# Kernel tuning notes

Measured on AMD Instinct MI355X. Metric: run time of the kernel, lower is better.

Reference implementation:

```python
import jax, jax.numpy as jnp
import numpy as np

B, T, C, HID, K, H = 8, 1024, 512, 2048, 31, 4  # batch, time, in_chans, hidden_chans, kernel, wshare


def setup_inputs() -> dict:
    key = jax.random.key(0)
    ks = jax.random.split(key, 8)
    n = lambda k_, sh, sc: jax.random.normal(k_, sh, dtype=jnp.float32) * sc
    return {
        "x": n(ks[0], (B, T, C), 1.0),
        "Wl": n(ks[1], (H * K, C), 0.05),      # linear_weight.weight
        "bl": n(ks[2], (H * K,), 0.01),          # linear_weight.bias
        "bias": n(ks[3], (C,), 0.02),            # self.bias
        "Wc": n(ks[4], (HID, C, K), 0.01),       # pointwise_conv1.weight (O,I,K)
        "bc": n(ks[5], (HID,), 0.01),            # pointwise_conv1.bias
        "W2": n(ks[6], (C, HID), 0.01),          # w_2.weight
        "b2": n(ks[7], (C,), 0.01),              # w_2.bias
    }


def reference(x, Wl, bl, bias, Wc, bc, W2, b2):
    Bq, Tq, Cq = x.shape
    d = Cq // H  # channels per weight-share head
    # dynamic conv logits: (B,T,H,K)
    logits = (x @ Wl.T + bl).reshape(Bq, Tq, H, K)
    # banded positions: output t attends to t + j - (K-1)//2
    offs = jnp.arange(K) - (K - 1) // 2
    pos = jnp.arange(Tq)[:, None] + offs[None, :]          # (T,K)
    valid = (pos >= 0) & (pos < Tq)
    logits = jnp.where(valid[None, :, None, :], logits, -jnp.inf)
    w = jax.nn.softmax(logits, axis=-1)                     # softmax over window (matches banded softmax over T)
    # gather windowed inputs: (B,T,K,H,d)
    xg = x.reshape(Bq, Tq, H, d)[:, jnp.clip(pos, 0, Tq - 1)]
    y = jnp.einsum('bthk,btkhd->bthd', w, xg).reshape(Bq, Tq, Cq)
    # (B,C,T) + bias
    y = y.transpose(0, 2, 1) + bias[None, :, None]
    # pointwise_conv1: Conv1d(C->HID, kernel K, padding 0) -> T' = T-K+1
    z = jax.lax.conv_general_dilated(y, Wc, (1,), 'VALID',
                                     dimension_numbers=('NCH', 'OIH', 'NCH'))
    z = z + bc[None, :, None]
    z = jax.nn.selu(z.transpose(0, 2, 1))                   # (B,T',HID)
    return z @ W2.T + b2                                    # (B,T',C)
```

## Files before the change

### kernel.cpp

```cpp
#include <hip/hip_runtime.h>
#include <hip/hip_bf16.h>

typedef __attribute__((ext_vector_type(8))) short short8;
typedef __attribute__((ext_vector_type(4))) float f32x4;

#define NB 8
#define NT 1024
#define NC 512
#define NHID 2048
#define NK 31
#define NH 4
#define NTP 994
#define MROWS (NB * NTP)
#define TG 4

__device__ __forceinline__ void gload_lds16(const void* g, void* l) {
  __builtin_amdgcn_global_load_lds(
      (const __attribute__((address_space(1))) void*)g,
      (__attribute__((address_space(3))) void*)l, 16, 0, 0);
}

__global__ __launch_bounds__(256) void prep_wc(const float* __restrict__ Wc,
                                               __hip_bfloat16* __restrict__ Wt) {
  const int blk = blockIdx.x;
  const int cb = blk & 7;
  const int o0 = (blk >> 3) << 3;
  const int c0 = cb << 6;
  const int obig = o0 >> 8;
  const int orb = o0 & 255;
  __shared__ float lds[8 * 64 * NK];
  for (int ol = 0; ol < 8; ++ol) {
    const float* src = Wc + ((size_t)(o0 + ol) * NC + c0) * NK;
    for (int i = threadIdx.x; i < 64 * NK; i += 256) lds[ol * (64 * NK) + i] = src[i];
  }
  __syncthreads();
  for (int i = threadIdx.x; i < NK * 8 * 64; i += 256) {
    const int k = i >> 9;
    const int rem = i & 511;
    const int ol = rem >> 6;
    const int ci = rem & 63;
    Wt[((size_t)((obig * 8 + cb) * NK + k) << 14) + ((orb + ol) << 6) + (ci ^ (ol << 3))] =
        __float2bfloat16(lds[ol * (64 * NK) + ci * NK + k]);
  }
}

__global__ __launch_bounds__(256) void prep_w2(const float* __restrict__ W2,
                                               __hip_bfloat16* __restrict__ W2t) {
  const int i = blockIdx.x * 256 + threadIdx.x;
  if (i < 32 * 512 * 64) {
    const int oi = i & 63;
    const int c = (i >> 6) & 511;
    const int kb = i >> 15;
    const size_t dst = ((size_t)(((c >> 7) * 32 + kb) * 128 + (c & 127)) << 6) +
                       (oi ^ ((c & 7) << 3));
    W2t[dst] = __float2bfloat16(W2[(size_t)c * NHID + (kb << 6) + oi]);
  }
}

__global__ __launch_bounds__(256) void dynconv(const float* __restrict__ x,
                                               const float* __restrict__ Wl,
                                               const float* __restrict__ bl,
                                               const float* __restrict__ bias,
                                               __hip_bfloat16* __restrict__ Y) {
  const int t0 = blockIdx.x * TG;
  const int b = blockIdx.y;
  const int tid = threadIdx.x, lane = tid & 63, w = tid >> 6;
  __shared__ float xt[TG][NC];
  __shared__ float lg[TG][NH * NK];
  __shared__ float wsm[TG][NH][NK];

  for (int i = tid; i < TG * NC; i += 256) {
    const int tg = i >> 9, c = i & 511;
    xt[tg][c] = x[((size_t)b * NT + t0 + tg) * NC + c];
  }
  __syncthreads();

  for (int i = 0; i < 31; ++i) {
    const int id = (i << 2) | w;
    const float* wrow = Wl + (size_t)id * NC + (lane << 3);
    float wv[8];
#pragma unroll
    for (int u = 0; u < 8; ++u) wv[u] = wrow[u];
    const float blv = bl[id];
#pragma unroll
    for (int tg = 0; tg < TG; ++tg) {
      float s = 0.f;
#pragma unroll
      for (int u = 0; u < 8; ++u) s += xt[tg][(lane << 3) + u] * wv[u];
#pragma unroll
      for (int off = 32; off; off >>= 1) s += __shfl_xor(s, off);
      if (lane == 0) lg[tg][id] = s + blv;
    }
  }
  __syncthreads();

  if (tid < TG * NH) {
    const int tg = tid >> 2, h = tid & 3;
    const int t = t0 + tg;
    int jlo = 15 - t; if (jlo < 0) jlo = 0;
    int jhi = 1038 - t; if (jhi > 30) jhi = 30;
    float mx = -1e30f;
    for (int j = jlo; j <= jhi; ++j) mx = fmaxf(mx, lg[tg][h * NK + j]);
    float ssum = 0.f;
    for (int j = 0; j < NK; ++j) {
      const float e = (j >= jlo && j <= jhi) ? __expf(lg[tg][h * NK + j] - mx) : 0.f;
      wsm[tg][h][j] = e;
      ssum += e;
    }
    const float inv = 1.f / ssum;
    for (int j = 0; j < NK; ++j) wsm[tg][h][j] *= inv;
  }
  __syncthreads();

  const int c = tid << 1;
  const int h = c >> 7;
  const float2* x2 = (const float2*)x;
  const float bias0 = bias[c], bias1 = bias[c + 1];
#pragma unroll
  for (int tg = 0; tg < TG; ++tg) {
    const int t = t0 + tg;
    float a0 = 0.f, a1 = 0.f;
#pragma unroll
    for (int j = 0; j < NK; ++j) {
      int pos = t + j - 15;
      pos = pos < 0 ? 0 : (pos > NT - 1 ? NT - 1 : pos);
      const float wgt = wsm[tg][h][j];
      const float2 v = x2[(((size_t)b * NT + pos) << 8) + tid];
      a0 += wgt * v.x;
      a1 += wgt * v.y;
    }
    const int cs = (c & ~63) | ((c & 63) ^ ((t & 7) << 3));
    __hip_bfloat162 hv;
    hv.x = __float2bfloat16(a0 + bias0);
    hv.y = __float2bfloat16(a1 + bias1);
    *(__hip_bfloat162*)(Y + ((size_t)b * NT + t) * NC + cs) = hv;
  }
}

__global__ __launch_bounds__(512, 2) void conv_gemm(const __hip_bfloat16* __restrict__ Y,
                                                    const __hip_bfloat16* __restrict__ Wt,
                                                    const float* __restrict__ bc,
                                                    __hip_bfloat16* __restrict__ Z) {
  const int o0 = blockIdx.x << 8;
  const int t0 = blockIdx.y << 8;
  const int b = blockIdx.z;
  __shared__ __align__(16) __hip_bfloat16 Ys[288 * 64];
  __shared__ __align__(16) __hip_bfloat16 Bs[2][256 * 64];
  const int tid = threadIdx.x;
  const int lane = tid & 63, wid = tid >> 6;
  const int wr = wid >> 2, wcid = wid & 3;
  const int obig = o0 >> 8;

  f32x4 acc[8][4] = {};

  auto stageY = [&](int cb_) {
    const int c0 = cb_ << 6;
#pragma unroll
    for (int p = 0; p < 5; ++p) {
      const int i = (p << 9) + tid;
      if (i < 2304) {
        int grow = t0 + (i >> 3);
        if (grow > NT - 1) grow = NT - 1;
        gload_lds16(Y + (((size_t)b * NT + grow) << 9) + c0 + ((i & 7) << 3),
                    &Ys[i << 3]);
      }
    }
  };
  auto stageB = [&](int bufi, int s_) {
    const __hip_bfloat16* wb = Wt + (((size_t)(obig * 248 + s_)) << 14);
#pragma unroll
    for (int p = 0; p < 4; ++p) {
      const int i = (p << 9) + tid;
      gload_lds16(wb + (i << 3), &Bs[bufi][i << 3]);
    }
  };

  stageY(0);
  stageB(0, 0);

  int buf = 0;
  for (int cb = 0; cb < 8; ++cb) {
    for (int k = 0; k < NK; ++k) {
      const int s = cb * 31 + k;
      if (s < 247) {
        stageB(buf ^ 1, s + 1);
        asm volatile("s_waitcnt vmcnt(4)" ::: "memory");
      } else {
        asm volatile("s_waitcnt vmcnt(0)" ::: "memory");
      }
      __builtin_amdgcn_sched_barrier(0);
      __builtin_amdgcn_s_barrier();
      __builtin_amdgcn_sched_barrier(0);

      __builtin_amdgcn_s_setprio(1);
#pragma unroll
      for (int kk = 0; kk < 2; ++kk) {
        const int ko = (kk << 5) + ((lane >> 4) << 3);
        short8 av[8], bv[4];
#pragma unroll
        for (int m = 0; m < 8; ++m) {
          const int r2 = (wr << 7) + (m << 4) + (lane & 15) + k;
          av[m] = *(const short8*)&Ys[(r2 << 6) + (ko ^ ((r2 & 7) << 3))];
        }
#pragma unroll
        for (int n = 0; n < 4; ++n) {
          const int br = (wcid << 6) + (n << 4) + (lane & 15);
          bv[n] = *(const short8*)&Bs[buf][(br << 6) + (ko ^ ((br & 7) << 3))];
        }
#pragma unroll
        for (int m = 0; m < 8; ++m)
#pragma unroll
          for (int n = 0; n < 4; ++n)
            acc[m][n] = __builtin_amdgcn_mfma_f32_16x16x32_bf16(av[m], bv[n], acc[m][n], 0, 0, 0);
      }
      __builtin_amdgcn_s_setprio(0);

      __builtin_amdgcn_sched_barrier(0);
      __builtin_amdgcn_s_barrier();
      __builtin_amdgcn_sched_barrier(0);
      buf ^= 1;
    }
    if (cb < 7) stageY(cb + 1);
  }

  const float kS = 1.0507009873554805f;
  const float kAS = 1.7580993408473766f;
#pragma unroll
  for (int n = 0; n < 4; ++n) {
    const int col = o0 + (wcid << 6) + (n << 4) + (lane & 15);
    const float bcv = bc[col];
#pragma unroll
    for (int m = 0; m < 8; ++m) {
      const int rbase = (wr << 7) + (m << 4) + ((lane >> 4) << 2);
#pragma unroll
      for (int r = 0; r < 4; ++r) {
        const int tp = t0 + rbase + r;
        if (tp < NTP) {
          const float v = acc[m][n][r] + bcv;
          const float s = v > 0.f ? kS * v : kAS * (__expf(v) - 1.f);
          const size_t grow = (size_t)b * NTP + tp;
          const int cs = (col & ~63) | ((col & 63) ^ (((int)(grow & 7)) << 3));
          Z[grow * NHID + cs] = __float2bfloat16(s);
        }
      }
    }
  }
}

__global__ __launch_bounds__(256) void out_gemm(const __hip_bfloat16* __restrict__ Zm,
                                                const __hip_bfloat16* __restrict__ W2t,
                                                const float* __restrict__ b2,
                                                float* __restrict__ Out) {
  const int n0 = blockIdx.x << 7;
  const int m0 = blockIdx.y << 7;
  __shared__ __align__(16) __hip_bfloat16 As[128 * 64];
  __shared__ __align__(16) __hip_bfloat16 Bs[128 * 64];
  const int tid = threadIdx.x;
  const int lane = tid & 63, wid = tid >> 6;
  const int wr = wid >> 1, wc = wid & 1;

  f32x4 acc[4][4] = {};

  for (int kb = 0; kb < 32; ++kb) {
#pragma unroll
    for (int p = 0; p < 4; ++p) {
      const int i = (p << 8) + tid;
      int row = m0 + (i >> 3);
      if (row > MROWS - 1) row = MROWS - 1;
      gload_lds16(Zm + ((size_t)row << 11) + (kb << 6) + ((i & 7) << 3), &As[i << 3]);
    }
    const __hip_bfloat16* wb = W2t + ((size_t)((n0 >> 7) * 32 + kb) << 13);
#pragma unroll
    for (int p = 0; p < 4; ++p) {
      const int i = (p << 8) + tid;
      gload_lds16(wb + (i << 3), &Bs[i << 3]);
    }
    __syncthreads();
#pragma unroll
    for (int kk = 0; kk < 2; ++kk) {
      const int ko = (kk << 5) + ((lane >> 4) << 3);
      short8 av[4], bv[4];
#pragma unroll
      for (int m = 0; m < 4; ++m) {
        const int r = (wr << 6) + (m << 4) + (lane & 15);
        av[m] = *(const short8*)&As[(r << 6) + (ko ^ ((r & 7) << 3))];
      }
#pragma unroll
      for (int n = 0; n < 4; ++n) {
        const int br = (wc << 6) + (n << 4) + (lane & 15);
        bv[n] = *(const short8*)&Bs[(br << 6) + (ko ^ ((br & 7) << 3))];
      }
#pragma unroll
      for (int m = 0; m < 4; ++m)
#pragma unroll
        for (int n = 0; n < 4; ++n)
          acc[m][n] = __builtin_amdgcn_mfma_f32_16x16x32_bf16(av[m], bv[n], acc[m][n], 0, 0, 0);
    }
    __syncthreads();
  }

#pragma unroll
  for (int n = 0; n < 4; ++n) {
    const int col = n0 + (wc << 6) + (n << 4) + (lane & 15);
    const float b2v = b2[col];
#pragma unroll
    for (int m = 0; m < 4; ++m) {
      const int rbase = m0 + (wr << 6) + (m << 4) + ((lane >> 4) << 2);
#pragma unroll
      for (int r = 0; r < 4; ++r) {
        const int row = rbase + r;
        if (row < MROWS) Out[(size_t)row * NC + col] = acc[m][n][r] + b2v;
      }
    }
  }
}

extern "C" void kernel_launch(void* const* d_in, const int* in_sizes, int n_in,
                              void* d_out, int out_size, void* d_ws, size_t ws_size,
                              hipStream_t stream) {
  const float* x = (const float*)d_in[0];
  const float* Wl = (const float*)d_in[1];
  const float* bl = (const float*)d_in[2];
  const float* bias = (const float*)d_in[3];
  const float* Wc = (const float*)d_in[4];
  const float* bc = (const float*)d_in[5];
  const float* W2 = (const float*)d_in[6];
  const float* b2 = (const float*)d_in[7];
  float* out = (float*)d_out;

  char* ws = (char*)d_ws;
  __hip_bfloat16* Wt = (__hip_bfloat16*)(ws);
  __hip_bfloat16* Y = (__hip_bfloat16*)(ws + 65011712);
  __hip_bfloat16* W2t = (__hip_bfloat16*)(ws + 73400320);
  __hip_bfloat16* Z = (__hip_bfloat16*)(ws + 75497472);

  hipLaunchKernelGGL(prep_wc, dim3(2048), dim3(256), 0, stream, Wc, Wt);
  hipLaunchKernelGGL(prep_w2, dim3(4096), dim3(256), 0, stream, W2, W2t);
  hipLaunchKernelGGL(dynconv, dim3(NT / TG, NB), dim3(256), 0, stream, x, Wl, bl, bias, Y);
  hipLaunchKernelGGL(conv_gemm, dim3(NHID / 256, 4, NB), dim3(512), 0, stream, Y, Wt, bc, Z);
  hipLaunchKernelGGL(out_gemm, dim3(NC / 128, (MROWS + 127) / 128), dim3(256), 0, stream,
                     Z, W2t, b2, out);
}
```

Baseline: 707.5 us.

## Triple-buffer weight tiles and split MFMA loop into four interleaved quadrant phases

The conv GEMM moves from double to triple buffering of the weight tile, prefetching two steps ahead. Each k-step is split into four quadrant phases, each with its own LDS fragment loads, MFMA batch and barrier, and the four global-to-LDS copies of the next tile are spread across those phases. The aim is to hide global-load latency and overlap LDS reads with MFMA work while using fewer live fragment registers. In exchange it adds many more barriers per step and an extra 32KB of LDS, which may limit occupancy at two blocks per CU.

```diff
diff --git a/kernel.cpp b/kernel.cpp
--- a/kernel.cpp
+++ b/kernel.cpp
@@ -19,6 +19,18 @@
       (const __attribute__((address_space(1))) void*)g,
       (__attribute__((address_space(3))) void*)l, 16, 0, 0);
 }
+
+#define BARX()                                  \
+  do {                                          \
+    __builtin_amdgcn_sched_barrier(0);          \
+    __builtin_amdgcn_s_barrier();               \
+    __builtin_amdgcn_sched_barrier(0);          \
+  } while (0)
+#define LGKM0()                                          \
+  do {                                                   \
+    asm volatile("s_waitcnt lgkmcnt(0)" ::: "memory");   \
+    __builtin_amdgcn_sched_barrier(0);                   \
+  } while (0)
 
 __global__ __launch_bounds__(256) void prep_wc(const float* __restrict__ Wc,
                                                __hip_bfloat16* __restrict__ Wt) {
@@ -145,7 +157,7 @@
   const int t0 = blockIdx.y << 8;
   const int b = blockIdx.z;
   __shared__ __align__(16) __hip_bfloat16 Ys[288 * 64];
-  __shared__ __align__(16) __hip_bfloat16 Bs[2][256 * 64];
+  __shared__ __align__(16) __hip_bfloat16 Bsm[3][256 * 64];
   const int tid = threadIdx.x;
   const int lane = tid & 63, wid = tid >> 6;
   const int wr = wid >> 2, wcid = wid & 3;
@@ -166,59 +178,130 @@
       }
     }
   };
-  auto stageB = [&](int bufi, int s_) {
+  auto stageBc = [&](__hip_bfloat16* dst, int s_, int p) {
     const __hip_bfloat16* wb = Wt + (((size_t)(obig * 248 + s_)) << 14);
-#pragma unroll
-    for (int p = 0; p < 4; ++p) {
-      const int i = (p << 9) + tid;
-      gload_lds16(wb + (i << 3), &Bs[bufi][i << 3]);
-    }
+    const int i = (p << 9) + tid;
+    gload_lds16(wb + (i << 3), dst + (i << 3));
   };
 
+  __hip_bfloat16* b0 = Bsm[0];
+  __hip_bfloat16* b1 = Bsm[1];
+  __hip_bfloat16* b2 = Bsm[2];
+
   stageY(0);
-  stageB(0, 0);
-
-  int buf = 0;
+#pragma unroll
+  for (int p = 0; p < 4; ++p) stageBc(b0, 0, p);
+#pragma unroll
+  for (int p = 0; p < 4; ++p) stageBc(b1, 1, p);
+
+  short8 av[2][4];
+  short8 bv[2][2][2];
+
+  const int l15 = lane & 15;
+  const int kob = (lane >> 4) << 3;
+
   for (int cb = 0; cb < 8; ++cb) {
     for (int k = 0; k < NK; ++k) {
       const int s = cb * 31 + k;
-      if (s < 247) {
-        stageB(buf ^ 1, s + 1);
+      const bool st = (s <= 245);
+      if ((k == 0 && s > 0) || s == 247) {
+        asm volatile("s_waitcnt vmcnt(0)" ::: "memory");
+      } else {
         asm volatile("s_waitcnt vmcnt(4)" ::: "memory");
-      } else {
-        asm volatile("s_waitcnt vmcnt(0)" ::: "memory");
-      }
-      __builtin_amdgcn_sched_barrier(0);
-      __builtin_amdgcn_s_barrier();
-      __builtin_amdgcn_sched_barrier(0);
-
+      }
+      BARX();
+
+      if (st) stageBc(b2, s + 2, 0);
+#pragma unroll
+      for (int kk = 0; kk < 2; ++kk) {
+        const int ko = (kk << 5) + kob;
+#pragma unroll
+        for (int m = 0; m < 4; ++m) {
+          const int r2 = (wr << 7) + (m << 4) + l15 + k;
+          av[kk][m] = *(const short8*)&Ys[(r2 << 6) + (ko ^ ((r2 & 7) << 3))];
+        }
+#pragma unroll
+        for (int n = 0; n < 2; ++n) {
+          const int br = (wcid << 6) + (n << 4) + l15;
+          bv[kk][0][n] = *(const short8*)&b0[(br << 6) + (ko ^ ((br & 7) << 3))];
+        }
+      }
+      BARX();
+      LGKM0();
       __builtin_amdgcn_s_setprio(1);
 #pragma unroll
+      for (int kk = 0; kk < 2; ++kk)
+#pragma unroll
+        for (int m = 0; m < 4; ++m)
+#pragma unroll
+          for (int n = 0; n < 2; ++n)
+            acc[m][n] = __builtin_amdgcn_mfma_f32_16x16x32_bf16(av[kk][m], bv[kk][0][n],
+                                                                acc[m][n], 0, 0, 0);
+      __builtin_amdgcn_s_setprio(0);
+      BARX();
+
+      if (st) stageBc(b2, s + 2, 1);
+#pragma unroll
       for (int kk = 0; kk < 2; ++kk) {
-        const int ko = (kk << 5) + ((lane >> 4) << 3);
-        short8 av[8], bv[4];
-#pragma unroll
-        for (int m = 0; m < 8; ++m) {
-          const int r2 = (wr << 7) + (m << 4) + (lane & 15) + k;
-          av[m] = *(const short8*)&Ys[(r2 << 6) + (ko ^ ((r2 & 7) << 3))];
+        const int ko = (kk << 5) + kob;
+#pragma unroll
+        for (int n = 0; n < 2; ++n) {
+          const int br = (wcid << 6) + 32 + (n << 4) + l15;
+          bv[kk][1][n] = *(const short8*)&b0[(br << 6) + (ko ^ ((br & 7) << 3))];
         }
-#pragma unroll
-        for (int n = 0; n < 4; ++n) {
-          const int br = (wcid << 6) + (n << 4) + (lane & 15);
-          bv[n] = *(const short8*)&Bs[buf][(br << 6) + (ko ^ ((br & 7) << 3))];
+      }
+      BARX();
+      LGKM0();
+      __builtin_amdgcn_s_setprio(1);
+#pragma unroll
+      for (int kk = 0; kk < 2; ++kk)
+#pragma unroll
+        for (int m = 0; m < 4; ++m)
+#pragma unroll
+          for (int n = 0; n < 2; ++n)
+            acc[m][2 + n] = __builtin_amdgcn_mfma_f32_16x16x32_bf16(av[kk][m], bv[kk][1][n],
+                                                                    acc[m][2 + n], 0, 0, 0);
+      __builtin_amdgcn_s_setprio(0);
+      BARX();
+
+      if (st) stageBc(b2, s + 2, 2);
+#pragma unroll
+      for (int kk = 0; kk < 2; ++kk) {
+        const int ko = (kk << 5) + kob;
+#pragma unroll
+        for (int m = 0; m < 4; ++m) {
+          const int r2 = (wr << 7) + 64 + (m << 4) + l15 + k;
+          av[kk][m] = *(const short8*)&Ys[(r2 << 6) + (ko ^ ((r2 & 7) << 3))];
         }
-#pragma unroll
-        for (int m = 0; m < 8; ++m)
-#pragma unroll
-          for (int n = 0; n < 4; ++n)
-            acc[m][n] = __builtin_amdgcn_mfma_f32_16x16x32_bf16(av[m], bv[n], acc[m][n], 0, 0, 0);
-      }
+      }
+      BARX();
+      LGKM0();
+      __builtin_amdgcn_s_setprio(1);
+#pragma unroll
+      for (int kk = 0; kk < 2; ++kk)
+#pragma unroll
+        for (int m = 0; m < 4; ++m)
+#pragma unroll
+          for (int n = 0; n < 2; ++n)
+            acc[4 + m][2 + n] = __builtin_amdgcn_mfma_f32_16x16x32_bf16(
+                av[kk][m], bv[kk][1][n], acc[4 + m][2 + n], 0, 0, 0);
       __builtin_amdgcn_s_setprio(0);
-
-      __builtin_amdgcn_sched_barrier(0);
-      __builtin_amdgcn_s_barrier();
-      __builtin_amdgcn_sched_barrier(0);
-      buf ^= 1;
+      BARX();
+
+      if (st) stageBc(b2, s + 2, 3);
+      __builtin_amdgcn_s_setprio(1);
+#pragma unroll
+      for (int kk = 0; kk < 2; ++kk)
+#pragma unroll
+        for (int m = 0; m < 4; ++m)
+#pragma unroll
+          for (int n = 0; n < 2; ++n)
+            acc[4 + m][n] = __builtin_amdgcn_mfma_f32_16x16x32_bf16(
+                av[kk][m], bv[kk][0][n], acc[4 + m][n], 0, 0, 0);
+      __builtin_amdgcn_s_setprio(0);
+      BARX();
+
+      __hip_bfloat16* tp = b0; b0 = b1; b1 = b2; b2 = tp;
     }
     if (cb < 7) stageY(cb + 1);
   }
```

Measured after the change: 711.6 us. About the same (+0.6%).
